# Kernel optimization log

Measured on AMD Instinct MI355X. Metric: run time of the kernel, lower is better.

Reference implementation:

```python
import jax, jax.numpy as jnp
import numpy as np

B, L, K, E, H, NH, W_OFF = 8, 512, 16, 32, 1, 64, 1
DK = E // H


def setup_inputs() -> dict:
    key = jax.random.key(0)
    ks = jax.random.split(key, 12)
    return {
        "time_steps": jax.random.uniform(ks[0], (B, L), jnp.float32),
        "val": jax.random.normal(ks[1], (B, L), jnp.float32),
        "mark": jax.random.randint(ks[2], (B, L), 1, K + 1, dtype=jnp.int32),
        "non_pad_mask": jnp.ones((B, L, 1), jnp.float32),
        "Wl": jax.random.normal(ks[3], (1, 1), jnp.float32) * 0.5,
        "bl": jnp.zeros((1,), jnp.float32),
        "Wp": jax.random.normal(ks[4], (E - 1, 1), jnp.float32) * 0.5,
        "bp": jnp.zeros((E - 1,), jnp.float32),
        "Wq": jax.random.normal(ks[5], (E, E), jnp.float32) / np.sqrt(E).astype(np.float32),
        "bq": jnp.zeros((E,), jnp.float32),
        "Wk": jax.random.normal(ks[6], (E, E), jnp.float32) / np.sqrt(E).astype(np.float32),
        "bk": jnp.zeros((E,), jnp.float32),
        "Wo": jax.random.normal(ks[7], (NH, K * H), jnp.float32) / np.sqrt(K * H).astype(np.float32),
        "bo": jnp.zeros((NH,), jnp.float32),
        "W_ih": jax.random.normal(ks[8], (3 * NH, NH), jnp.float32) / np.sqrt(NH).astype(np.float32),
        "W_hh": jax.random.normal(ks[9], (3 * NH, NH), jnp.float32) / np.sqrt(NH).astype(np.float32),
        "b_ih": jnp.zeros((3 * NH,), jnp.float32),
        "b_hh": jnp.zeros((3 * NH,), jnp.float32),
    }


def _forward(time_steps, val, mark, non_pad_mask,
             Wl, bl, Wp, bp, Wq, bq, Wk, bk, Wo, bo,
             W_ih, W_hh, b_ih, b_hh):
    # transform_to_3d_ts: scatter each (b,l) event into its channel mark-1
    npm = non_pad_mask[:, :, 0]                       # [B,L]
    onehot = (mark - 1)[:, :, None] == jnp.arange(K)[None, None, :]  # [B,L,K]
    valid = onehot & (npm > 0)[:, :, None]
    val_blk = jnp.where(valid, val[:, :, None], 0.0)          # [B,L,K]
    mask_blk = jnp.where(valid, npm[:, :, None], 0.0)         # [B,L,K]

    # learn_time_embedding
    tt = time_steps[:, :, None]                                # [B,L,1]
    key_emb = jnp.concatenate([tt @ Wl.T + bl, jnp.sin(tt @ Wp.T + bp)], axis=-1)  # [B,L,E]

    # subsequent mask (tril with diag offset w)
    att_mask = jnp.tril(jnp.ones((L, L), jnp.float32), W_OFF)  # [L,L]

    # multiTimeAttention (query == key == key_emb)
    q = (key_emb @ Wq.T + bq).reshape(B, L, H, DK).transpose(0, 2, 1, 3)  # [B,H,L,DK]
    k = (key_emb @ Wk.T + bk).reshape(B, L, H, DK).transpose(0, 2, 1, 3)
    scores = jnp.einsum('bhqd,bhkd->bhqk', q, k) / jnp.sqrt(jnp.float32(DK))  # [B,H,L,L]
    # broadcast to [B,H,L,L,K] (repeat_interleave equivalent), apply att_mask then pad mask
    scores5 = scores[..., None] * att_mask[None, None, :, :, None]
    scores5 = jnp.where(mask_blk[:, None, None, :, :] == 0, -1e9, scores5)
    p_attn = jax.nn.softmax(scores5, axis=-2)                  # softmax over key positions
    x = jnp.sum(p_attn * val_blk[:, None, None, :, :], axis=-2)  # [B,H,L,K]
    x = x.transpose(0, 2, 1, 3).reshape(B, L, H * K)
    att_out = x @ Wo.T + bo                                    # [B,L,NH]

    # single-layer GRU over time (PyTorch gate equations)
    def step(h, xt):
        gi = xt @ W_ih.T + b_ih
        gh = h @ W_hh.T + b_hh
        ir, iz, inn = jnp.split(gi, 3, axis=-1)
        hr, hz, hn = jnp.split(gh, 3, axis=-1)
        r = jax.nn.sigmoid(ir + hr)
        z = jax.nn.sigmoid(iz + hz)
        n = jnp.tanh(inn + r * hn)
        h_new = (1.0 - z) * n + z * h
        return h_new, h_new

    h0 = jnp.zeros((B, NH), att_out.dtype)
    _, outs = jax.lax.scan(step, h0, att_out.transpose(1, 0, 2))  # [L,B,NH]
    return outs.transpose(1, 0, 2)                                # [B,L,NH]


def reference(time_steps, val, mark, non_pad_mask,
              Wl, bl, Wp, bp, Wq, bq, Wk, bk, Wo, bo,
              W_ih, W_hh, b_ih, b_hh):
    return _forward(time_steps, val, mark, non_pad_mask,
                    Wl, bl, Wp, bp, Wq, bq, Wk, bk, Wo, bo,
                    W_ih, W_hh, b_ih, b_hh)
```

## Files before the change

kernel.cpp:

```cpp
#include <hip/hip_runtime.h>
#include <math.h>

#define B_    8
#define L_    512
#define K_    16
#define E_    32
#define NH_   64
#define WOFF_ 1


typedef float v2f __attribute__((ext_vector_type(2)));
typedef float v4f __attribute__((ext_vector_type(4)));

__global__ __launch_bounds__(256) void k_embed(
    const float* __restrict__ ts, const float* __restrict__ Wl,
    const float* __restrict__ bl, const float* __restrict__ Wp,
    const float* __restrict__ bp, const float* __restrict__ Wq,
    const float* __restrict__ bq, const float* __restrict__ Wk,
    const float* __restrict__ bk,
    float* __restrict__ qmat, float* __restrict__ kmatT)
{
    __shared__ float WqL[1024], WkL[1024];
    __shared__ float bqL[32], bkL[32], WpL[31], bpL[31];
    __shared__ float wl0, bl0;
    const int tid = threadIdx.x;

    {
        float4 v = ((const float4*)Wq)[tid];
        ((float4*)WqL)[tid] = v;
        float4 u = ((const float4*)Wk)[tid];
        ((float4*)WkL)[tid] = u;
    }
    if (tid < 32) { bqL[tid] = bq[tid]; bkL[tid] = bk[tid]; }
    if (tid < 31) { WpL[tid] = Wp[tid]; bpL[tid] = bp[tid]; }
    if (tid == 0) { wl0 = Wl[0]; bl0 = bl[0]; }
    __syncthreads();

    const int p = blockIdx.x * 256 + tid;
    const float t = ts[p];
    float e[32];
    e[0] = t * wl0 + bl0;
    #pragma unroll
    for (int j = 1; j < 32; ++j) e[j] = sinf(t * WpL[j - 1] + bpL[j - 1]);

    const int b = p >> 9, l = p & 511;
    float4* qm4 = (float4*)(qmat + (size_t)p * 32);
    float*  kT  = kmatT + (size_t)b * 32 * 512 + l;

    for (int dq = 0; dq < 8; ++dq) {
        float q0 = bqL[4*dq+0], q1 = bqL[4*dq+1], q2 = bqL[4*dq+2], q3 = bqL[4*dq+3];
        float k0 = bkL[4*dq+0], k1 = bkL[4*dq+1], k2 = bkL[4*dq+2], k3 = bkL[4*dq+3];
        const float* wq = &WqL[(4*dq) * 32];
        const float* wk = &WkL[(4*dq) * 32];
        #pragma unroll
        for (int j = 0; j < 32; ++j) {
            const float ej = e[j];
            q0 = fmaf(wq[j],      ej, q0);
            q1 = fmaf(wq[32 + j], ej, q1);
            q2 = fmaf(wq[64 + j], ej, q2);
            q3 = fmaf(wq[96 + j], ej, q3);
            k0 = fmaf(wk[j],      ej, k0);
            k1 = fmaf(wk[32 + j], ej, k1);
            k2 = fmaf(wk[64 + j], ej, k2);
            k3 = fmaf(wk[96 + j], ej, k3);
        }
        qm4[dq] = make_float4(q0, q1, q2, q3);
        kT[(4*dq + 0) * 512] = k0;
        kT[(4*dq + 1) * 512] = k1;
        kT[(4*dq + 2) * 512] = k2;
        kT[(4*dq + 3) * 512] = k3;
    }
}

__global__ __launch_bounds__(256) void k_attn_gi(
    const float* __restrict__ qmat, const float* __restrict__ kmatT,
    const float* __restrict__ val,  const int*   __restrict__ mark,
    const float* __restrict__ npm,  const float* __restrict__ Wo,
    const float* __restrict__ bo,   const float* __restrict__ Wih,
    const float* __restrict__ bih,  float* __restrict__ gi)
{
    __shared__ float srow[4 * 512];
    __shared__ int   cc[512];
    __shared__ float vv[512];
    __shared__ float attL[4 * 64];
    const int tid = threadIdx.x;
    const int qb  = blockIdx.x;
    const int b   = blockIdx.y;
    const int qb0 = qb * 4;

    for (int k = tid; k < 512; k += 256) {
        const int   m  = mark[b * 512 + k];
        const float np = npm[b * 512 + k];
        cc[k] = (np > 0.0f) ? (m - 1) : -1;
        vv[k] = val[b * 512 + k];
    }
    __syncthreads();

    const int w = tid >> 6, lane = tid & 63;
    const float* kTb = kmatT + (size_t)b * 32 * 512;
    const int q = qb0 + w;

    {
        float qr[32];
        const float4* qm4 = (const float4*)(qmat + (size_t)(b * 512 + q) * 32);
        #pragma unroll
        for (int j4 = 0; j4 < 8; ++j4) {
            float4 v = qm4[j4];
            qr[4*j4+0] = v.x; qr[4*j4+1] = v.y; qr[4*j4+2] = v.z; qr[4*j4+3] = v.w;
        }

        float acc[8];
        #pragma unroll
        for (int m = 0; m < 8; ++m) acc[m] = 0.0f;
        #pragma unroll 4
        for (int j = 0; j < 32; ++j) {
            const float* row = kTb + j * 512 + lane;
            const float  qj  = qr[j];
            #pragma unroll
            for (int m = 0; m < 8; ++m) acc[m] = fmaf(qj, row[m * 64], acc[m]);
        }
        #pragma unroll
        for (int m = 0; m < 8; ++m)
            srow[w * 512 + m * 64 + lane] = acc[m] * 0.17677669529663687f;

        const int c = lane & 15, s = lane >> 4;
        float mx = -1e30f, Z = 0.0f, X = 0.0f;
        const int base = s * 128;
        for (int t = 0; t < 128; ++t) {
            const int k = base + ((t + s) & 127);
            if (cc[k] == c) {
                const float l  = (k <= q + WOFF_) ? srow[w * 512 + k] : 0.0f;
                const float mn = fmaxf(mx, l);
                const float e1 = __expf(l - mn);
                const float sc = __expf(mx - mn);
                Z = Z * sc + e1;
                X = X * sc + e1 * vv[k];
                mx = mn;
            }
        }
        #pragma unroll
        for (int off = 16; off <= 32; off <<= 1) {
            const float mo = __shfl_xor(mx, off);
            const float Zo = __shfl_xor(Z, off);
            const float Xo = __shfl_xor(X, off);
            const float mn = fmaxf(mx, mo);
            const float a0 = __expf(mx - mn);
            const float a1 = __expf(mo - mn);
            Z = Z * a0 + Zo * a1;
            X = X * a0 + Xo * a1;
            mx = mn;
        }
        const float x = (Z > 0.0f) ? X / Z : 0.0f;

        float xs[16];
        #pragma unroll
        for (int c2 = 0; c2 < 16; ++c2) xs[c2] = __shfl(x, c2);

        const float4* wo4 = (const float4*)(Wo + lane * 16);
        float a = bo[lane];
        #pragma unroll
        for (int c4 = 0; c4 < 4; ++c4) {
            float4 v = wo4[c4];
            a += xs[4*c4+0] * v.x + xs[4*c4+1] * v.y + xs[4*c4+2] * v.z + xs[4*c4+3] * v.w;
        }
        attL[w * 64 + lane] = a;
    }
    __syncthreads();

    const size_t out0 = (size_t)(b * 512 + qb0) * 192;
    for (int pp = 0; pp < 3; ++pp) {
        const int p = tid + 256 * pp;
        const int r = p / 192, g = p - r * 192;
        float a0 = bih[g], a1 = 0.f, a2 = 0.f, a3 = 0.f;
        const float* wrow = Wih + g * 64;
        const float* arow = &attL[r * 64];
        #pragma unroll
        for (int j = 0; j < 64; j += 4) {
            a0 = fmaf(arow[j + 0], wrow[j + 0], a0);
            a1 = fmaf(arow[j + 1], wrow[j + 1], a1);
            a2 = fmaf(arow[j + 2], wrow[j + 2], a2);
            a3 = fmaf(arow[j + 3], wrow[j + 3], a3);
        }
        gi[out0 + p] = (a0 + a1) + (a2 + a3);
    }
}


#define GRU_STEP(u, DO_REFILL) {                                           \
    v4f hv[16];                                                            \
    _Pragma("unroll")                                                      \
    for (int k = 0; k < 6; ++k) hv[k] = hs4[k];                            \
    const float gr = pr[u], gz = pz[u], gn = pn[u];                        \
    if (DO_REFILL) {                                                       \
        pr[u] = pf[0];                                                     \
        pz[u] = pf[64];                                                    \
        pn[u] = pf[128];                                                   \
        pf += 192;                                                         \
    }                                                                      \
    v2f ar2 = {gr + br, 0.0f};                                             \
    v2f az2 = {gz + bz, 0.0f};                                             \
    v2f an2 = {bn, 0.0f};                                                  \
    _Pragma("unroll")                                                      \
    for (int k = 0; k < 16; ++k) {                                         \
        if (k < 10) hv[k + 6] = hs4[k + 6];                                \
        v2f p0 = __builtin_shufflevector(hv[k], hv[k], 0, 1);              \
        v2f p1 = __builtin_shufflevector(hv[k], hv[k], 2, 3);              \
        ar2 = wr[2*k]     * p0 + ar2;                                      \
        az2 = wz[2*k]     * p0 + az2;                                      \
        an2 = wn[2*k]     * p0 + an2;                                      \
        ar2 = wr[2*k + 1] * p1 + ar2;                                      \
        az2 = wz[2*k + 1] * p1 + az2;                                      \
        an2 = wn[2*k + 1] * p1 + an2;                                      \
    }                                                                      \
    const float ar = ar2.x + ar2.y;                                        \
    const float az = az2.x + az2.y;                                        \
    const float hn = an2.x + an2.y;                                        \
    const float r = __builtin_amdgcn_rcpf(1.0f + __expf(-ar));             \
    const float z = __builtin_amdgcn_rcpf(1.0f + __expf(-az));             \
    float npre = gn + r * hn;                                              \
    npre = fminf(fmaxf(npre, -15.0f), 15.0f);                              \
    const float e2 = __expf(2.0f * npre);                                  \
    const float n  = (e2 - 1.0f) * __builtin_amdgcn_rcpf(e2 + 1.0f);       \
    h = fmaf(z, h - n, n);                                                 \
    hs[lane] = h;                                                          \
    *outp = h;                                                             \
    outp += 64;                                                            \
}

__global__ __launch_bounds__(64, 1) void k_gru(
    const float* __restrict__ gi, const float* __restrict__ Whh,
    const float* __restrict__ bhh, float* __restrict__ out)
{
    __shared__ float hs[64];
    const int lane = threadIdx.x;
    const int b    = blockIdx.x;

    v2f wr[32], wz[32], wn[32];
    {
        const v2f* r2 = (const v2f*)(Whh + (size_t)lane * 64);
        const v2f* z2 = (const v2f*)(Whh + (size_t)(lane + 64) * 64);
        const v2f* n2 = (const v2f*)(Whh + (size_t)(lane + 128) * 64);
        #pragma unroll
        for (int j = 0; j < 32; ++j) {
            wr[j] = r2[j];
            wz[j] = z2[j];
            wn[j] = n2[j];
        }
    }
    const float br = bhh[lane];
    const float bz = bhh[lane + 64];
    const float bn = bhh[lane + 128];

    const float* gib  = gi  + (size_t)b * 512 * 192;
    float*       outp = out + (size_t)b * 512 * 64 + lane;

    float h = 0.0f;
    hs[lane] = 0.0f;

    float pr[2], pz[2], pn[2];
    #pragma unroll
    for (int i = 0; i < 2; ++i) {
        const float* gp = gib + (size_t)i * 192;
        pr[i] = gp[lane];
        pz[i] = gp[lane + 64];
        pn[i] = gp[lane + 128];
    }
    const float* pf = gib + (size_t)2 * 192 + lane;

    const v4f* hs4 = (const v4f*)hs;

    for (int tt = 0; tt < 510; tt += 2) {
        GRU_STEP(0, 1)
        GRU_STEP(1, 1)
    }
    GRU_STEP(0, 0)
    GRU_STEP(1, 0)
}

extern "C" void kernel_launch(void* const* d_in, const int* in_sizes, int n_in,
                              void* d_out, int out_size, void* d_ws, size_t ws_size,
                              hipStream_t stream)
{
    const float* ts   = (const float*)d_in[0];
    const float* val  = (const float*)d_in[1];
    const int*   mark = (const int*)  d_in[2];
    const float* npm  = (const float*)d_in[3];
    const float* Wl   = (const float*)d_in[4];
    const float* bl   = (const float*)d_in[5];
    const float* Wp   = (const float*)d_in[6];
    const float* bp   = (const float*)d_in[7];
    const float* Wq   = (const float*)d_in[8];
    const float* bq   = (const float*)d_in[9];
    const float* Wk   = (const float*)d_in[10];
    const float* bk   = (const float*)d_in[11];
    const float* Wo   = (const float*)d_in[12];
    const float* bo   = (const float*)d_in[13];
    const float* Wih  = (const float*)d_in[14];
    const float* Whh  = (const float*)d_in[15];
    const float* bih  = (const float*)d_in[16];
    const float* bhh  = (const float*)d_in[17];

    float* ws    = (float*)d_ws;
    float* qmat  = ws;
    float* kmatT = ws + 131072;
    float* gi    = ws + 524288;
    float* out   = (float*)d_out;

    k_embed<<<16, 256, 0, stream>>>(ts, Wl, bl, Wp, bp, Wq, bq, Wk, bk, qmat, kmatT);
    k_attn_gi<<<dim3(128, 8), 256, 0, stream>>>(qmat, kmatT, val, mark, npm,
                                                Wo, bo, Wih, bih, gi);
    k_gru<<<8, 64, 0, stream>>>(gi, Whh, bhh, out);
}
```

Measured before the change: 327.7 us.

## Split GRU gate matvecs across three wavefronts with LDS exchange and barrier

The GRU kernel now runs 192 threads per batch instead of 64: each wavefront computes one gate's recurrent matvec (r, z or n) with its own weight row in registers. The partial gate sums are exchanged through shared memory behind a workgroup barrier, and each wave keeps its own copy of the hidden state to avoid a second barrier. This cuts the serial FMA chain per step to a third, at the cost of one barrier and LDS round trip per time step. The double-buffered gx array guards against races between consecutive steps.

```diff
diff --git a/kernel.cpp b/kernel.cpp
--- a/kernel.cpp
+++ b/kernel.cpp
@@ -186,95 +186,93 @@
 }
 
 
-#define GRU_STEP(u, DO_REFILL) {                                           \
+#define GRU3_STEP(u, DO_REFILL) {                                          \
+       \
     v4f hv[16];                                                            \
     _Pragma("unroll")                                                      \
-    for (int k = 0; k < 6; ++k) hv[k] = hs4[k];                            \
-    const float gr = pr[u], gz = pz[u], gn = pn[u];                        \
+    for (int k = 0; k < 16; ++k) hv[k] = hs4[k];                           \
+    const float gown = pown[u];                                            \
+    const float gnv  = pgn[u];                                             \
     if (DO_REFILL) {                                                       \
-        pr[u] = pf[0];                                                     \
-        pz[u] = pf[64];                                                    \
-        pn[u] = pf[128];                                                   \
+        pown[u] = pf[ownOff];       \
+        pgn[u]  = pf[gnOff];                                               \
         pf += 192;                                                         \
     }                                                                      \
-    v2f ar2 = {gr + br, 0.0f};                                             \
-    v2f az2 = {gz + bz, 0.0f};                                             \
-    v2f an2 = {bn, 0.0f};                                                  \
+       \
+    v2f a2 = {(g == 2) ? bown : (gown + bown), 0.0f};                      \
     _Pragma("unroll")                                                      \
     for (int k = 0; k < 16; ++k) {                                         \
-        if (k < 10) hv[k + 6] = hs4[k + 6];                                \
         v2f p0 = __builtin_shufflevector(hv[k], hv[k], 0, 1);              \
         v2f p1 = __builtin_shufflevector(hv[k], hv[k], 2, 3);              \
-        ar2 = wr[2*k]     * p0 + ar2;                                      \
-        az2 = wz[2*k]     * p0 + az2;                                      \
-        an2 = wn[2*k]     * p0 + an2;                                      \
-        ar2 = wr[2*k + 1] * p1 + ar2;                                      \
-        az2 = wz[2*k + 1] * p1 + az2;                                      \
-        an2 = wn[2*k + 1] * p1 + an2;                                      \
+        a2 = wg[2*k]     * p0 + a2;                                        \
+        a2 = wg[2*k + 1] * p1 + a2;                                        \
     }                                                                      \
-    const float ar = ar2.x + ar2.y;                                        \
-    const float az = az2.x + az2.y;                                        \
-    const float hn = an2.x + an2.y;                                        \
-    const float r = __builtin_amdgcn_rcpf(1.0f + __expf(-ar));             \
-    const float z = __builtin_amdgcn_rcpf(1.0f + __expf(-az));             \
-    float npre = gn + r * hn;                                              \
+    gx[u][g][lane] = a2.x + a2.y;                                          \
+          \
+    asm volatile("s_waitcnt lgkmcnt(0)" ::: "memory");                     \
+    __builtin_amdgcn_sched_barrier(0);                                     \
+    __builtin_amdgcn_s_barrier();                                          \
+    __builtin_amdgcn_sched_barrier(0);                                     \
+    const float arS = gx[u][0][lane];                                      \
+    const float azS = gx[u][1][lane];                                      \
+    const float hnS = gx[u][2][lane];                                      \
+     \
+    const float r = __builtin_amdgcn_rcpf(1.0f + __expf(-arS));            \
+    const float z = __builtin_amdgcn_rcpf(1.0f + __expf(-azS));            \
+    float npre = gnv + r * hnS;                                            \
     npre = fminf(fmaxf(npre, -15.0f), 15.0f);                              \
     const float e2 = __expf(2.0f * npre);                                  \
     const float n  = (e2 - 1.0f) * __builtin_amdgcn_rcpf(e2 + 1.0f);       \
     h = fmaf(z, h - n, n);                                                 \
-    hs[lane] = h;                                                          \
-    *outp = h;                                                             \
+    hsw_g[lane] = h;                       \
+    if (g == 2) *outp = h;                     \
     outp += 64;                                                            \
 }
 
-__global__ __launch_bounds__(64, 1) void k_gru(
+__global__ __launch_bounds__(192, 1) void k_gru(
     const float* __restrict__ gi, const float* __restrict__ Whh,
     const float* __restrict__ bhh, float* __restrict__ out)
 {
-    __shared__ float hs[64];
-    const int lane = threadIdx.x;
+    __shared__ float hsw[3][64];
+    __shared__ float gx[2][3][64];
+    const int tid  = threadIdx.x;
+    const int lane = tid & 63;
+    const int g    = tid >> 6;
     const int b    = blockIdx.x;
 
-    v2f wr[32], wz[32], wn[32];
+    v2f wg[32];
     {
-        const v2f* r2 = (const v2f*)(Whh + (size_t)lane * 64);
-        const v2f* z2 = (const v2f*)(Whh + (size_t)(lane + 64) * 64);
-        const v2f* n2 = (const v2f*)(Whh + (size_t)(lane + 128) * 64);
-        #pragma unroll
-        for (int j = 0; j < 32; ++j) {
-            wr[j] = r2[j];
-            wz[j] = z2[j];
-            wn[j] = n2[j];
-        }
-    }
-    const float br = bhh[lane];
-    const float bz = bhh[lane + 64];
-    const float bn = bhh[lane + 128];
+        const v2f* w2 = (const v2f*)(Whh + (size_t)(g * 64 + lane) * 64);
+        #pragma unroll
+        for (int j = 0; j < 32; ++j) wg[j] = w2[j];
+    }
+    const float bown = bhh[g * 64 + lane];
 
     const float* gib  = gi  + (size_t)b * 512 * 192;
     float*       outp = out + (size_t)b * 512 * 64 + lane;
 
+    float* hsw_g = hsw[g];
     float h = 0.0f;
-    hs[lane] = 0.0f;
-
-    float pr[2], pz[2], pn[2];
+    hsw_g[lane] = 0.0f;
+
+    const int ownOff = g * 64 + lane;
+    const int gnOff  = 128 + lane;
+    float pown[2], pgn[2];
     #pragma unroll
     for (int i = 0; i < 2; ++i) {
-        const float* gp = gib + (size_t)i * 192;
-        pr[i] = gp[lane];
-        pz[i] = gp[lane + 64];
-        pn[i] = gp[lane + 128];
-    }
-    const float* pf = gib + (size_t)2 * 192 + lane;
-
-    const v4f* hs4 = (const v4f*)hs;
+        pown[i] = gib[i * 192 + ownOff];
+        pgn[i]  = gib[i * 192 + gnOff];
+    }
+    const float* pf = gib + 2 * 192;
+
+    const v4f* hs4 = (const v4f*)hsw_g;
 
     for (int tt = 0; tt < 510; tt += 2) {
-        GRU_STEP(0, 1)
-        GRU_STEP(1, 1)
-    }
-    GRU_STEP(0, 0)
-    GRU_STEP(1, 0)
+        GRU3_STEP(0, 1)
+        GRU3_STEP(1, 1)
+    }
+    GRU3_STEP(0, 0)
+    GRU3_STEP(1, 0)
 }
 
 extern "C" void kernel_launch(void* const* d_in, const int* in_sizes, int n_in,
@@ -309,5 +307,5 @@
     k_embed<<<16, 256, 0, stream>>>(ts, Wl, bl, Wp, bp, Wq, bq, Wk, bk, qmat, kmatT);
     k_attn_gi<<<dim3(128, 8), 256, 0, stream>>>(qmat, kmatT, val, mark, npm,
                                                 Wo, bo, Wih, bih, gi);
-    k_gru<<<8, 64, 0, stream>>>(gi, Whh, bhh, out);
-}
+    k_gru<<<8, 192, 0, stream>>>(gi, Whh, bhh, out);
+}
```

New measurement: 376.3 us. 1.15x slower.

## Precompute per-channel key index lists to skip non-matching keys in attention

Applied to the files above, without the earlier changes.

The embed kernel now builds, for each batch, channel and key segment, a compact byte list of the key positions whose mark matches that channel. The attention kernel loads these lists into shared memory and walks only the matching keys, instead of scanning all 128 keys per segment with a branch. This removes roughly 15/16 of the divergent loop iterations in the online softmax. In exchange it adds a serial list-building loop in the embed kernel and an extra global-to-shared copy of the lists.

```diff
diff --git a/kernel.cpp b/kernel.cpp
--- a/kernel.cpp
+++ b/kernel.cpp
@@ -17,8 +17,10 @@
     const float* __restrict__ bl, const float* __restrict__ Wp,
     const float* __restrict__ bp, const float* __restrict__ Wq,
     const float* __restrict__ bq, const float* __restrict__ Wk,
-    const float* __restrict__ bk,
-    float* __restrict__ qmat, float* __restrict__ kmatT)
+    const float* __restrict__ bk, const int* __restrict__ mark,
+    const float* __restrict__ npm,
+    float* __restrict__ qmat, float* __restrict__ kmatT,
+    unsigned char* __restrict__ lists, int* __restrict__ counts)
 {
     __shared__ float WqL[1024], WkL[1024];
     __shared__ float bqL[32], bkL[32], WpL[31], bpL[31];
@@ -70,30 +72,53 @@
         kT[(4*dq + 2) * 512] = k2;
         kT[(4*dq + 3) * 512] = k3;
     }
+
+    if ((blockIdx.x & 1) == 0 && tid < 64) {
+        const int bb = blockIdx.x >> 1;
+        const int c  = tid & 15, s = tid >> 4;
+        const int row = c * 4 + s;
+        unsigned char* myl = lists + (size_t)((bb * 64 + row) << 7);
+        int cnt = 0;
+        for (int tt2 = 0; tt2 < 128; ++tt2) {
+            const int j = (tt2 + s) & 127;
+            const int k = s * 128 + j;
+            const int   m  = mark[bb * 512 + k];
+            const float np = npm[bb * 512 + k];
+            const int cck = (np > 0.0f) ? (m - 1) : -1;
+            if (cck == c) { myl[cnt] = (unsigned char)j; ++cnt; }
+        }
+        counts[bb * 64 + row] = cnt;
+    }
 }
 
 __global__ __launch_bounds__(256) void k_attn_gi(
     const float* __restrict__ qmat, const float* __restrict__ kmatT,
-    const float* __restrict__ val,  const int*   __restrict__ mark,
-    const float* __restrict__ npm,  const float* __restrict__ Wo,
+    const float* __restrict__ val,  const unsigned char* __restrict__ lists,
+    const int* __restrict__ counts, const float* __restrict__ Wo,
     const float* __restrict__ bo,   const float* __restrict__ Wih,
     const float* __restrict__ bih,  float* __restrict__ gi)
 {
     __shared__ float srow[4 * 512];
-    __shared__ int   cc[512];
     __shared__ float vv[512];
     __shared__ float attL[4 * 64];
+    __shared__ unsigned char listsL[64 * 132];
+    __shared__ int countsL[64];
     const int tid = threadIdx.x;
     const int qb  = blockIdx.x;
     const int b   = blockIdx.y;
     const int qb0 = qb * 4;
 
-    for (int k = tid; k < 512; k += 256) {
-        const int   m  = mark[b * 512 + k];
-        const float np = npm[b * 512 + k];
-        cc[k] = (np > 0.0f) ? (m - 1) : -1;
+    for (int k = tid; k < 512; k += 256)
         vv[k] = val[b * 512 + k];
-    }
+    {
+        const unsigned int* gsrc = (const unsigned int*)(lists + ((size_t)b << 13));
+        unsigned int* ldst = (unsigned int*)listsL;
+        for (int idx = tid; idx < 2048; idx += 256) {
+            const int c4s = idx >> 5, wrd = idx & 31;
+            ldst[c4s * 33 + wrd] = gsrc[idx];
+        }
+    }
+    if (tid < 64) countsL[tid] = counts[b * 64 + tid];
     __syncthreads();
 
     const int w = tid >> 6, lane = tid & 63;
@@ -124,19 +149,20 @@
             srow[w * 512 + m * 64 + lane] = acc[m] * 0.17677669529663687f;
 
         const int c = lane & 15, s = lane >> 4;
+        const int base = s * 128;
+        const int nc = countsL[c * 4 + s];
+        const unsigned char* myl = &listsL[(c * 4 + s) * 132];
         float mx = -1e30f, Z = 0.0f, X = 0.0f;
-        const int base = s * 128;
-        for (int t = 0; t < 128; ++t) {
-            const int k = base + ((t + s) & 127);
-            if (cc[k] == c) {
-                const float l  = (k <= q + WOFF_) ? srow[w * 512 + k] : 0.0f;
-                const float mn = fmaxf(mx, l);
-                const float e1 = __expf(l - mn);
-                const float sc = __expf(mx - mn);
-                Z = Z * sc + e1;
-                X = X * sc + e1 * vv[k];
-                mx = mn;
-            }
+        for (int i = 0; i < nc; ++i) {
+            const int j = myl[i];
+            const int k = base + j;
+            const float l  = (k <= q + WOFF_) ? srow[w * 512 + k] : 0.0f;
+            const float mn = fmaxf(mx, l);
+            const float e1 = __expf(l - mn);
+            const float sc = __expf(mx - mn);
+            Z = Z * sc + e1;
+            X = X * sc + e1 * vv[k];
+            mx = mn;
         }
         #pragma unroll
         for (int off = 16; off <= 32; off <<= 1) {
@@ -303,11 +329,14 @@
     float* ws    = (float*)d_ws;
     float* qmat  = ws;
     float* kmatT = ws + 131072;
+    unsigned char* lists = (unsigned char*)(ws + 262144);
+    int*   counts = (int*)(ws + 393216);
     float* gi    = ws + 524288;
     float* out   = (float*)d_out;
 
-    k_embed<<<16, 256, 0, stream>>>(ts, Wl, bl, Wp, bp, Wq, bq, Wk, bk, qmat, kmatT);
-    k_attn_gi<<<dim3(128, 8), 256, 0, stream>>>(qmat, kmatT, val, mark, npm,
+    k_embed<<<16, 256, 0, stream>>>(ts, Wl, bl, Wp, bp, Wq, bq, Wk, bk,
+                                    mark, npm, qmat, kmatT, lists, counts);
+    k_attn_gi<<<dim3(128, 8), 256, 0, stream>>>(qmat, kmatT, val, lists, counts,
                                                 Wo, bo, Wih, bih, gi);
     k_gru<<<8, 64, 0, stream>>>(gi, Whh, bhh, out);
 }
```

Measured after the change: 338.2 us. 1.03x slower.
